# Kernel optimization log

Measured on AMD Instinct MI355X. Metric: run time of the kernel, lower is better.

The kernel has to match this reference:

```python
import jax, jax.numpy as jnp
import numpy as np

B, S, D, H = 2, 512, 1024, 8
DK = D // H
DFF = 4 * D
R = 51
SEP = 64


def setup_inputs() -> dict:
    key = jax.random.key(0)
    ks = jax.random.split(key, 12)
    def w(k, shape, scale=0.02):
        return jax.random.normal(k, shape, jnp.float32) * scale
    return {
        "x": jax.random.normal(ks[0], (B, S, D), jnp.float32),
        "relation": jax.random.randint(ks[1], (B, S, S), 0, R),
        "mask": jnp.ones((B, S, S), jnp.int32),
        "sep_id": SEP,
        "history_reg": jnp.ones((1,), jnp.float32),
        "Wq": w(ks[2], (D, D)), "bq": jnp.zeros((D,), jnp.float32),
        "Wk": w(ks[3], (D, D)), "bk": jnp.zeros((D,), jnp.float32),
        "Wv": w(ks[4], (D, D)), "bv": jnp.zeros((D,), jnp.float32),
        "Wo": w(ks[5], (D, D)), "bo": jnp.zeros((D,), jnp.float32),
        "rel_k_emb": w(ks[6], (R, DK)),
        "rel_v_emb": w(ks[7], (R, DK)),
        "ln1_g": jnp.ones((D,), jnp.float32), "ln1_b": jnp.zeros((D,), jnp.float32),
        "ln2_g": jnp.ones((D,), jnp.float32), "ln2_b": jnp.zeros((D,), jnp.float32),
        "W1": w(ks[8], (D, DFF)), "b1": jnp.zeros((DFF,), jnp.float32),
        "W2": w(ks[9], (DFF, D)), "b2": jnp.zeros((D,), jnp.float32),
    }


def _layer_norm(x, g, b, eps=1e-5):
    m = jnp.mean(x, axis=-1, keepdims=True)
    v = jnp.mean(jnp.square(x - m), axis=-1, keepdims=True)
    return (x - m) * jax.lax.rsqrt(v + eps) * g + b


def _forward(x, relation, mask, sep_id, history_reg, Wq, bq, Wk, bk, Wv, bv, Wo, bo,
             rel_k_emb, rel_v_emb, ln1_g, ln1_b, ln2_g, ln2_b, W1, b1, W2, b2):
    b, s, d = x.shape
    # relation-aware self-attention sublayer (pre-norm)
    h = _layer_norm(x, ln1_g, ln1_b)
    rk = rel_k_emb[relation]  # [B,S,S,DK]
    rv = rel_v_emb[relation]  # [B,S,S,DK]
    def proj(W, bias):
        return (h @ W + bias).reshape(b, s, H, DK).transpose(0, 2, 1, 3)  # [B,H,S,DK]
    q, k, v = proj(Wq, bq), proj(Wk, bk), proj(Wv, bv)
    scores = jnp.einsum("bhid,bhjd->bhij", q, k) + jnp.einsum("bhid,bijd->bhij", q, rk)
    scores = scores / jnp.sqrt(jnp.float32(DK))
    scores = jnp.where(mask[:, None, :, :] == 0, jnp.float32(-1e9), scores)
    attn = jax.nn.softmax(scores, axis=-1)  # [B,H,S,S]
    ctx = jnp.einsum("bhij,bhjd->bhid", attn, v) + jnp.einsum("bhij,bijd->bhid", attn, rv)
    ctx = ctx.transpose(0, 2, 1, 3).reshape(b, s, d)
    attn_out = ctx @ Wo + bo
    # history regularization loss: attention mass on history tokens (positions < sep_id)
    loss = history_reg[0] * jnp.mean(attn[:, :, :, :sep_id])
    x = x + attn_out
    # FFN sublayer (pre-norm)
    h2 = _layer_norm(x, ln2_g, ln2_b)
    ffn = jax.nn.relu(h2 @ W1 + b1) @ W2 + b2
    x = x + ffn
    return x, loss


def reference(x, relation, mask, sep_id, history_reg, Wq, bq, Wk, bk, Wv, bv, Wo, bo,
              rel_k_emb, rel_v_emb, ln1_g, ln1_b, ln2_g, ln2_b, W1, b1, W2, b2):
    return _forward(x, relation, mask, sep_id, history_reg, Wq, bq, Wk, bk, Wv, bv,
                    Wo, bo, rel_k_emb, rel_v_emb, ln1_g, ln1_b, ln2_g, ln2_b,
                    W1, b1, W2, b2)
```

## Files before the change

### kernel.cpp

```cpp
#include <hip/hip_runtime.h>
#include <hip/hip_bf16.h>

#define NB 2
#define NS 512
#define ND 1024
#define NH 8
#define NDK 128
#define NDFF 4096
#define RPAD 64
#define LDSC 640
#define BSROWS 1024
#define NBH 16

typedef __bf16 bf16x8 __attribute__((ext_vector_type(8)));
typedef __bf16 bf16x4 __attribute__((ext_vector_type(4)));
typedef float f32x4 __attribute__((ext_vector_type(4)));

#define BM 64
#define BN 64
#define BK 64

__device__ __forceinline__ void gload16(const void* g, void* l) {
    __builtin_amdgcn_global_load_lds(
        (const __attribute__((address_space(1))) void*)g,
        (__attribute__((address_space(3))) void*)l, 16, 0, 0);
}

__global__ __launch_bounds__(256, 4) void gemm64(
    const __bf16* __restrict__ A, const __bf16* __restrict__ Bt,
    const __bf16* __restrict__ Brel,
    float* __restrict__ Cf, __bf16* __restrict__ Cb,
    const float* __restrict__ bias,
    int Ksp, int lda, int ldb, int ldc,
    long sA, long sA2, int zdivA,
    long sB, long sB2, int zdivB,
    long sC, int nsplit, long sPart, int flags)
{
    __shared__ __bf16 As0[BM * BK];
    __shared__ __bf16 As1[BM * BK];
    __shared__ __bf16 Bs0[BN * BK];
    __shared__ __bf16 Bs1[BN * BK];

    const int z = blockIdx.z;
    const int bh = z / nsplit, sp = z - bh * nsplit;
    const long kbase = (long)sp * Ksp;
    A  += (long)(bh / zdivA) * sA + (long)(bh % zdivA) * sA2 + kbase;
    Bt += (long)(bh / zdivB) * sB + (long)(bh % zdivB) * sB2 + kbase;
    const long cbase = (long)bh * sC + (long)sp * sPart;

    const int tM = blockIdx.y * BM, tN = blockIdx.x * BN;
    const int t = threadIdx.x, lane = t & 63, w = t >> 6;
    const int wr = w >> 1, wc = w & 1;

    const __bf16* Bbase = Bt;
    int ldbx = ldb, tNB = tN;
    if ((flags & 4) && tN >= NS) { Bbase = Brel + kbase; ldbx = 128; tNB = tN - NS; }

    const int srow = lane >> 3;
    const int scolE = ((((lane & 7) << 4) ^ (srow << 4)) >> 1);

    const __bf16* gA = A + (long)(tM + srow) * lda + scolE;
    const __bf16* gB = Bbase + (long)(tNB + srow) * ldbx + scolE;

    f32x4 acc[2][2];
#pragma unroll
    for (int m = 0; m < 2; ++m)
#pragma unroll
        for (int n = 0; n < 2; ++n)
#pragma unroll
            for (int j = 0; j < 4; ++j) acc[m][n][j] = 0.f;

    const int r16 = lane & 15;
    const int kq = (lane >> 4) * 8;
    const int xorE = (r16 & 7) * 8;
    const int nt = Ksp / BK;

    auto STAGE = [&](__bf16* as, __bf16* bs, int k0) {
#pragma unroll
        for (int i = 0; i < 2; ++i) {
            const int rr = (w + i * 4) * 8;
            gload16(gA + (long)rr * lda + k0, (void*)&as[rr * BK]);
            gload16(gB + (long)rr * ldbx + k0, (void*)&bs[rr * BK]);
        }
    };
    auto COMPUTE = [&](const __bf16* as, const __bf16* bs) {
#pragma unroll
        for (int ks = 0; ks < 2; ++ks) {
            bf16x8 af[2], bv[2];
#pragma unroll
            for (int m = 0; m < 2; ++m)
                af[m] = *(const bf16x8*)&as[(wr * 32 + m * 16 + r16) * BK + ((ks * 32 + kq) ^ xorE)];
#pragma unroll
            for (int n = 0; n < 2; ++n)
                bv[n] = *(const bf16x8*)&bs[(wc * 32 + n * 16 + r16) * BK + ((ks * 32 + kq) ^ xorE)];
#pragma unroll
            for (int m = 0; m < 2; ++m)
#pragma unroll
                for (int n = 0; n < 2; ++n)
                    acc[m][n] = __builtin_amdgcn_mfma_f32_16x16x32_bf16(af[m], bv[n], acc[m][n], 0, 0, 0);
        }
    };

    STAGE(As0, Bs0, 0);
    STAGE(As1, Bs1, BK);
    for (int tt = 0; tt < nt; tt += 2) {
        asm volatile("s_waitcnt vmcnt(4)\n\ts_barrier" ::: "memory");
        COMPUTE(As0, Bs0);
        asm volatile("s_waitcnt lgkmcnt(0)\n\ts_barrier" ::: "memory");
        const bool more = (tt + 2 < nt);
        if (more) {
            STAGE(As0, Bs0, (tt + 2) * BK);
            asm volatile("s_waitcnt vmcnt(4)\n\ts_barrier" ::: "memory");
        } else {
            asm volatile("s_waitcnt vmcnt(0)\n\ts_barrier" ::: "memory");
        }
        COMPUTE(As1, Bs1);
        asm volatile("s_waitcnt lgkmcnt(0)\n\ts_barrier" ::: "memory");
        if (more) STAGE(As1, Bs1, (tt + 3) * BK);
    }

    const bool relu = (flags & 1) != 0;
#pragma unroll
    for (int m = 0; m < 2; ++m) {
        const int gr0 = tM + wr * 32 + m * 16 + (lane >> 4) * 4;
#pragma unroll
        for (int n = 0; n < 2; ++n) {
            const int gc = tN + wc * 32 + n * 16 + (lane & 15);
            const float bb = bias ? bias[gc] : 0.f;
#pragma unroll
            for (int j = 0; j < 4; ++j) {
                float v = acc[m][n][j] + bb;
                if (relu) v = fmaxf(v, 0.f);
                const long idx = cbase + (long)(gr0 + j) * ldc + gc;
                if (Cb) Cb[idx] = (__bf16)v;
                else Cf[idx] = v;
            }
        }
    }
}

__global__ __launch_bounds__(256) void ln_bf16(
    const float* __restrict__ x, const float* __restrict__ g,
    const float* __restrict__ bb, __bf16* __restrict__ out)
{
    const long row = blockIdx.x;
    const float* xr = x + row * ND;
    __bf16* orow = out + row * ND;
    const int t = threadIdx.x;
    float4 v = reinterpret_cast<const float4*>(xr)[t];
    float s = v.x + v.y + v.z + v.w;
    float s2 = v.x * v.x + v.y * v.y + v.z * v.z + v.w * v.w;
#pragma unroll
    for (int o = 32; o > 0; o >>= 1) {
        s += __shfl_xor(s, o, 64);
        s2 += __shfl_xor(s2, o, 64);
    }
    __shared__ float red[8];
    const int lane = t & 63, wv = t >> 6;
    if (lane == 0) { red[wv] = s; red[4 + wv] = s2; }
    __syncthreads();
    s = red[0] + red[1] + red[2] + red[3];
    s2 = red[4] + red[5] + red[6] + red[7];
    const float mean = s * (1.f / ND);
    const float var = s2 * (1.f / ND) - mean * mean;
    const float rs = rsqrtf(var + 1e-5f);
    const float xv[4] = {v.x, v.y, v.z, v.w};
    bf16x4 o;
#pragma unroll
    for (int j = 0; j < 4; ++j) {
        const int c = t * 4 + j;
        o[j] = (__bf16)((xv[j] - mean) * rs * g[c] + bb[c]);
    }
    *(bf16x4*)&orow[t * 4] = o;
}

__global__ void prep_weights(
    const float* __restrict__ Wq, const float* __restrict__ Wk,
    const float* __restrict__ Wv, const float* __restrict__ Wo,
    const float* __restrict__ W1, const float* __restrict__ W2,
    const float* __restrict__ relv,
    const float* __restrict__ bq, const float* __restrict__ bk,
    const float* __restrict__ bv, const float* __restrict__ relk,
    __bf16* __restrict__ WqkvT, __bf16* __restrict__ WoT,
    __bf16* __restrict__ W1T, __bf16* __restrict__ W2T,
    __bf16* __restrict__ relvT, float* __restrict__ biasqkv,
    __bf16* __restrict__ relkT, int R)
{
    const int tile = blockIdx.x;
    if (tile >= 12296) {
        const int ft = (tile - 12296) * 256 + threadIdx.y * 32 + threadIdx.x;
        if (ft < ND) biasqkv[ft] = bq[ft];
        else if (ft < 2 * ND) biasqkv[ft] = bk[ft - ND];
        else if (ft < 3 * ND) biasqkv[ft] = bv[ft - 2 * ND];
        else {
            const int idx = ft - 3 * ND;
            if (idx < 128 * NDK) {
                const int r = idx / NDK;
                relkT[idx] = (r < R) ? (__bf16)relk[idx] : (__bf16)0.f;
            }
        }
        return;
    }
    const float* src; __bf16* dst;
    int rows_in, cols_in, ldo, kx, ny;
    if (tile < 4096) {
        const int m = tile >> 10, r = tile & 1023;
        kx = r & 31; ny = r >> 5;
        rows_in = 1024; cols_in = 1024; ldo = 1024;
        src = m == 0 ? Wq : m == 1 ? Wk : m == 2 ? Wv : Wo;
        dst = m == 3 ? WoT : WqkvT + (size_t)m * 1024 * 1024;
    } else if (tile < 8192) {
        const int r = tile - 4096;
        kx = r & 31; ny = r >> 5;
        rows_in = 1024; cols_in = 4096; ldo = 1024; src = W1; dst = W1T;
    } else if (tile < 12288) {
        const int r = tile - 8192;
        kx = r & 127; ny = r >> 7;
        rows_in = 4096; cols_in = 1024; ldo = 4096; src = W2; dst = W2T;
    } else {
        const int r = tile - 12288;
        kx = r & 1; ny = r >> 1;
        rows_in = R; cols_in = 128; ldo = 64; src = relv; dst = relvT;
    }

    __shared__ float tl[32][33];
    const int k0 = kx * 32, n0 = ny * 32;
    const int tx = threadIdx.x, ty = threadIdx.y;
#pragma unroll
    for (int dy = 0; dy < 32; dy += 8) {
        const int k = k0 + ty + dy, n = n0 + tx;
        tl[ty + dy][tx] = (k < rows_in && n < cols_in) ? src[(long)k * cols_in + n] : 0.f;
    }
    __syncthreads();
#pragma unroll
    for (int dy = 0; dy < 32; dy += 8) {
        const int n = n0 + ty + dy, k = k0 + tx;
        if (n < cols_in && k < ldo) dst[(long)n * ldo + k] = (__bf16)tl[tx][ty + dy];
    }
}

__global__ void transpose_v(const __bf16* __restrict__ qkvb, __bf16* __restrict__ vt)
{
    __shared__ __bf16 tile[32][33];
    const int bh = blockIdx.z, b = bh >> 3, h = bh & 7;
    const int d0 = blockIdx.x * 32, i0 = blockIdx.y * 32;
    const int tx = threadIdx.x, ty = threadIdx.y;
    const __bf16* src = qkvb + 2 * ND + h * NDK;
#pragma unroll
    for (int dy = 0; dy < 32; dy += 8)
        tile[ty + dy][tx] = src[(long)(b * NS + i0 + ty + dy) * (3 * ND) + d0 + tx];
    __syncthreads();
#pragma unroll
    for (int dy = 0; dy < 32; dy += 8)
        vt[((long)bh * NDK + d0 + ty + dy) * NS + i0 + tx] = tile[tx][ty + dy];
}

__global__ __launch_bounds__(256) void softmax_rel(
    const __bf16* __restrict__ scores,
    const int* __restrict__ relation, const int* __restrict__ mask,
    __bf16* __restrict__ attn, __bf16* __restrict__ attnR,
    float* __restrict__ loss_part, const int* __restrict__ sep_p)
{
    const int i = blockIdx.x, b = blockIdx.y;
    const int t = threadIdx.x;
    const int* rrow = relation + ((long)b * NS + i) * NS;
    const int* mrow = mask + ((long)b * NS + i) * NS;
    const int r0 = rrow[t], r1 = rrow[t + 256];
    const int m0 = mrow[t], m1 = mrow[t + 256];
    const int sep = *sep_p;
    const int lane = t & 63, wv = t >> 6;

    __shared__ float qrl[RPAD];
    __shared__ float bins[RPAD];
    __shared__ float red[4];

    const float sc = 0.088388347648318447f;
    float lsum = 0.f;

#pragma unroll 1
    for (int h = 0; h < NH; ++h) {
        const long bh = (long)(b * NH + h);
        const __bf16* srow = scores + (bh * NS + i) * LDSC;
        __bf16* arow = attn + (bh * NS + i) * NS;
        __bf16* aRrow = attnR + (bh * NS + i) * RPAD;

        if (t < RPAD) { qrl[t] = (float)srow[NS + t]; bins[t] = 0.f; }
        __syncthreads();

        float v0 = ((float)srow[t] + qrl[r0]) * sc;
        float v1 = ((float)srow[t + 256] + qrl[r1]) * sc;
        if (m0 == 0) v0 = -1e9f;
        if (m1 == 0) v1 = -1e9f;

        float mx = fmaxf(v0, v1);
#pragma unroll
        for (int o = 32; o > 0; o >>= 1) mx = fmaxf(mx, __shfl_xor(mx, o, 64));
        if (lane == 0) red[wv] = mx;
        __syncthreads();
        mx = fmaxf(fmaxf(red[0], red[1]), fmaxf(red[2], red[3]));
        __syncthreads();

        const float e0 = __expf(v0 - mx), e1 = __expf(v1 - mx);
        float sm = e0 + e1;
#pragma unroll
        for (int o = 32; o > 0; o >>= 1) sm += __shfl_xor(sm, o, 64);
        if (lane == 0) red[wv] = sm;
        __syncthreads();
        sm = red[0] + red[1] + red[2] + red[3];

        const float inv = 1.f / sm;
        const float a0 = e0 * inv, a1 = e1 * inv;
        arow[t] = (__bf16)a0;
        arow[t + 256] = (__bf16)a1;
        atomicAdd(&bins[r0], a0);
        atomicAdd(&bins[r1], a1);
        if (t < sep) lsum += a0;
        if (t + 256 < sep) lsum += a1;
        __syncthreads();
        if (t < RPAD) aRrow[t] = (__bf16)bins[t];
        __syncthreads();
    }

#pragma unroll
    for (int o = 32; o > 0; o >>= 1) lsum += __shfl_xor(lsum, o, 64);
    if (lane == 0) red[wv] = lsum;
    __syncthreads();
    if (t == 0) loss_part[(long)b * NS + i] = red[0] + red[1] + red[2] + red[3];
}

__global__ __launch_bounds__(256) void ctx_reduce(
    const float* __restrict__ P, const __bf16* __restrict__ attnR,
    const __bf16* __restrict__ relvT, __bf16* __restrict__ ctxm)
{
    const int idx = blockIdx.x * 256 + threadIdx.x;
    const int d = idx & 127;
    const int i = (idx >> 7) & 511;
    const int h = (idx >> 16) & 7;
    const int b = idx >> 19;
    const long sP = (long)NBH * NS * NDK;
    float s = P[idx] + P[idx + sP];

    const bf16x8* ar = (const bf16x8*)(attnR + ((long)(idx >> 16) * NS + i) * RPAD);
    const bf16x8* rv = (const bf16x8*)(relvT + (long)d * RPAD);
    float acc = 0.f;
#pragma unroll
    for (int q = 0; q < 8; ++q) {
        bf16x8 a = ar[q], vv = rv[q];
#pragma unroll
        for (int j = 0; j < 8; ++j) acc += (float)a[j] * (float)vv[j];
    }
    ctxm[((long)(b * NS + i)) * ND + h * NDK + d] = (__bf16)(s + acc);
}

__global__ __launch_bounds__(256) void wo_reduce_ln(
    const float* __restrict__ P, const float* __restrict__ x,
    const float* __restrict__ bo, const float* __restrict__ g,
    const float* __restrict__ bb, float* __restrict__ out,
    __bf16* __restrict__ h2)
{
    const int row = blockIdx.x;
    const int t = threadIdx.x;
    const long i4 = (long)row * 256 + t;
    const long sP = (long)BSROWS * ND / 4;
    const float4* P4 = (const float4*)P;
    float4 s = P4[i4];
    const float4 t1 = P4[i4 + sP];
    s.x += t1.x; s.y += t1.y; s.z += t1.z; s.w += t1.w;
    const int col = t * 4;
    const float4 xv = ((const float4*)x)[i4];
    const float4 bv = *(const float4*)&bo[col];
    float4 o;
    o.x = s.x + xv.x + bv.x; o.y = s.y + xv.y + bv.y;
    o.z = s.z + xv.z + bv.z; o.w = s.w + xv.w + bv.w;
    ((float4*)out)[i4] = o;

    float sum = o.x + o.y + o.z + o.w;
    float sum2 = o.x * o.x + o.y * o.y + o.z * o.z + o.w * o.w;
#pragma unroll
    for (int of = 32; of > 0; of >>= 1) {
        sum += __shfl_xor(sum, of, 64);
        sum2 += __shfl_xor(sum2, of, 64);
    }
    __shared__ float red[8];
    const int lane = t & 63, wv = t >> 6;
    if (lane == 0) { red[wv] = sum; red[4 + wv] = sum2; }
    __syncthreads();
    sum = red[0] + red[1] + red[2] + red[3];
    sum2 = red[4] + red[5] + red[6] + red[7];
    const float mean = sum * (1.f / ND);
    const float var = sum2 * (1.f / ND) - mean * mean;
    const float rs = rsqrtf(var + 1e-5f);
    const float ov[4] = {o.x, o.y, o.z, o.w};
    bf16x4 hb;
#pragma unroll
    for (int j = 0; j < 4; ++j)
        hb[j] = (__bf16)((ov[j] - mean) * rs * g[col + j] + bb[col + j]);
    *(bf16x4*)&h2[(long)row * ND + col] = hb;
}

__global__ __launch_bounds__(256) void ffn2_reduce(
    const float* __restrict__ P, const float* __restrict__ b2, float* __restrict__ out,
    const float* __restrict__ loss_part, const float* __restrict__ hist,
    const int* __restrict__ sep_p, float* __restrict__ out_loss)
{
    const int i4 = blockIdx.x * 256 + threadIdx.x;
    const long sP = (long)BSROWS * ND / 4;
    const float4* P4 = (const float4*)P;
    float4 s = P4[i4];
    const float4 t1 = P4[i4 + sP];
    s.x += t1.x; s.y += t1.y; s.z += t1.z; s.w += t1.w;
    const int col = (i4 * 4) & (ND - 1);
    const float4 bv = *(const float4*)&b2[col];
    float4 o = ((float4*)out)[i4];
    o.x += s.x + bv.x; o.y += s.y + bv.y;
    o.z += s.z + bv.z; o.w += s.w + bv.w;
    ((float4*)out)[i4] = o;

    if (blockIdx.x == 0) {
        const int t = threadIdx.x;
        const float4 v = ((const float4*)loss_part)[t];
        float ls = v.x + v.y + v.z + v.w;
#pragma unroll
        for (int of = 32; of > 0; of >>= 1) ls += __shfl_xor(ls, of, 64);
        __shared__ float red[4];
        if ((t & 63) == 0) red[t >> 6] = ls;
        __syncthreads();
        if (t == 0) {
            const int sep = *sep_p;
            const float total = red[0] + red[1] + red[2] + red[3];
            const float denom = (float)NB * NH * NS * (float)(sep > 0 ? sep : 1);
            out_loss[0] = (sep > 0) ? hist[0] * total / denom : 0.f;
        }
    }
}

static inline int cdiv(int a, int b) { return (a + b - 1) / b; }

extern "C" void kernel_launch(void* const* d_in, const int* in_sizes, int n_in,
                              void* d_out, int out_size, void* d_ws, size_t ws_size,
                              hipStream_t stream)
{
    const float* x      = (const float*)d_in[0];
    const int* relation = (const int*)d_in[1];
    const int* mask     = (const int*)d_in[2];
    const int* sep_p    = (const int*)d_in[3];
    const float* hist   = (const float*)d_in[4];
    const float* Wq = (const float*)d_in[5],  *bq = (const float*)d_in[6];
    const float* Wk = (const float*)d_in[7],  *bk = (const float*)d_in[8];
    const float* Wv = (const float*)d_in[9],  *bv = (const float*)d_in[10];
    const float* Wo = (const float*)d_in[11], *bo = (const float*)d_in[12];
    const float* relk = (const float*)d_in[13];
    const float* relv = (const float*)d_in[14];
    const float* ln1g = (const float*)d_in[15], *ln1b = (const float*)d_in[16];
    const float* ln2g = (const float*)d_in[17], *ln2b = (const float*)d_in[18];
    const float* W1 = (const float*)d_in[19], *b1 = (const float*)d_in[20];
    const float* W2 = (const float*)d_in[21], *b2 = (const float*)d_in[22];
    const int R = in_sizes[13] / NDK;

    float* out = (float*)d_out;
    float* out_loss = out + (long)BSROWS * ND;

    char* p = (char*)d_ws;
    auto alloc = [&](size_t bytes) -> void* {
        void* r = (void*)p;
        p += (bytes + 255) & ~(size_t)255;
        return r;
    };
    __bf16* WqkvT   = (__bf16*)alloc((size_t)3 * ND * ND * 2);
    __bf16* WoT     = (__bf16*)alloc((size_t)ND * ND * 2);
    __bf16* W1T     = (__bf16*)alloc((size_t)NDFF * ND * 2);
    __bf16* W2T     = (__bf16*)alloc((size_t)ND * NDFF * 2);
    __bf16* relkT   = (__bf16*)alloc((size_t)128 * NDK * 2);
    __bf16* relvT   = (__bf16*)alloc((size_t)NDK * RPAD * 2);
    float*  biasqkv = (float*)alloc((size_t)3 * ND * 4);
    __bf16* h1      = (__bf16*)alloc((size_t)BSROWS * ND * 2);
    __bf16* qkvb    = (__bf16*)alloc((size_t)BSROWS * 3 * ND * 2);
    __bf16* vt      = (__bf16*)alloc((size_t)NBH * NDK * NS * 2);
    __bf16* attnb   = (__bf16*)alloc((size_t)NBH * NS * NS * 2);
    __bf16* attnR   = (__bf16*)alloc((size_t)NBH * NS * RPAD * 2);
    __bf16* ctxm    = (__bf16*)alloc((size_t)BSROWS * ND * 2);
    __bf16* h2      = (__bf16*)alloc((size_t)BSROWS * ND * 2);
    __bf16* F1      = (__bf16*)alloc((size_t)BSROWS * NDFF * 2);
    float*  loss_part = (float*)alloc((size_t)NB * NS * 4);
    float*  arena   = (float*)alloc((size_t)64 * 1024 * 1024);
    __bf16* scoresb = (__bf16*)arena;
    float* ctxPart  = arena + (size_t)3 * 1024 * 1024;
    float* woPart   = arena;
    float* f2Part   = arena + (size_t)2 * 1024 * 1024;

    const dim3 tb(32, 8);
    prep_weights<<<12372, tb, 0, stream>>>(Wq, Wk, Wv, Wo, W1, W2, relv,
                                           bq, bk, bv, relk,
                                           WqkvT, WoT, W1T, W2T, relvT,
                                           biasqkv, relkT, R);

    ln_bf16<<<BSROWS, 256, 0, stream>>>(x, ln1g, ln1b, h1);

    gemm64<<<dim3(48, 16, 1), 256, 0, stream>>>(
        h1, WqkvT, nullptr, nullptr, qkvb, biasqkv,
        ND, ND, ND, 3 * ND,
        0, 0, 1, 0, 0, 1, 0, 1, 0, 0);

    transpose_v<<<dim3(4, 16, NBH), tb, 0, stream>>>(qkvb, vt);

    gemm64<<<dim3(10, 8, NBH), 256, 0, stream>>>(
        qkvb, qkvb + ND, relkT, nullptr, scoresb, nullptr,
        NDK, 3 * ND, 3 * ND, LDSC,
        (long)NS * 3 * ND, NDK, NH,
        (long)NS * 3 * ND, NDK, NH,
        (long)NS * LDSC, 1, 0, 4);

    softmax_rel<<<dim3(NS, NB), 256, 0, stream>>>(
        scoresb, relation, mask, attnb, attnR, loss_part, sep_p);

    gemm64<<<dim3(2, 8, NBH * 2), 256, 0, stream>>>(
        attnb, vt, nullptr, ctxPart, nullptr, nullptr,
        256, NS, NS, NDK,
        (long)NS * NS, 0, 1,
        (long)NDK * NS, 0, 1,
        (long)NS * NDK, 2, (long)NBH * NS * NDK, 0);

    ctx_reduce<<<4096, 256, 0, stream>>>(ctxPart, attnR, relvT, ctxm);

    gemm64<<<dim3(16, 16, 2), 256, 0, stream>>>(
        ctxm, WoT, nullptr, woPart, nullptr, nullptr,
        512, ND, ND, ND,
        0, 0, 1, 0, 0, 1,
        0, 2, (long)BSROWS * ND, 0);

    wo_reduce_ln<<<BSROWS, 256, 0, stream>>>(woPart, x, bo, ln2g, ln2b, out, h2);

    gemm64<<<dim3(64, 16, 1), 256, 0, stream>>>(
        h2, W1T, nullptr, nullptr, F1, b1,
        ND, ND, ND, NDFF,
        0, 0, 1, 0, 0, 1, 0, 1, 0, 1);

    gemm64<<<dim3(16, 16, 2), 256, 0, stream>>>(
        F1, W2T, nullptr, f2Part, nullptr, nullptr,
        2048, NDFF, NDFF, ND,
        0, 0, 1, 0, 0, 1,
        0, 2, (long)BSROWS * ND, 0);

    ffn2_reduce<<<1024, 256, 0, stream>>>(f2Part, b2, out,
                                          loss_part, hist, sep_p, out_loss);
}
```

Baseline: 162.7 us.

## Fuse LN1 into prep kernel, remap GEMM blocks per XCD, raise MFMA priority

Folds the first layer norm into the weight-prep kernel as extra blocks, which removes one kernel launch. The GEMM's block index is remapped so consecutive logical tiles land on the same XCD, aiming for better L2 reuse on the multi-die MI355X. It also wraps the MFMA compute section in s_setprio to favour matrix issue. The remap adds integer division per block, and the fused prep kernel now shares its LDS layout between two different code paths.

```diff
diff --git a/kernel.cpp b/kernel.cpp
--- a/kernel.cpp
+++ b/kernel.cpp
@@ -41,14 +41,22 @@
     __shared__ __bf16 Bs0[BN * BK];
     __shared__ __bf16 Bs1[BN * BK];
 
-    const int z = blockIdx.z;
+    const unsigned gx = gridDim.x, gy = gridDim.y;
+    const unsigned n = gx * gy * gridDim.z;
+    const unsigned o = blockIdx.x + gx * (blockIdx.y + gy * blockIdx.z);
+    const unsigned q = n >> 3, r = n & 7, xcd = o & 7;
+    const unsigned nl = (xcd < r ? xcd * (q + 1) : r * (q + 1) + (xcd - r) * q) + (o >> 3);
+    const unsigned bx = nl % gx, tmp = nl / gx;
+    const unsigned by = tmp % gy, bz = tmp / gy;
+
+    const int z = bz;
     const int bh = z / nsplit, sp = z - bh * nsplit;
     const long kbase = (long)sp * Ksp;
     A  += (long)(bh / zdivA) * sA + (long)(bh % zdivA) * sA2 + kbase;
     Bt += (long)(bh / zdivB) * sB + (long)(bh % zdivB) * sB2 + kbase;
     const long cbase = (long)bh * sC + (long)sp * sPart;
 
-    const int tM = blockIdx.y * BM, tN = blockIdx.x * BN;
+    const int tM = by * BM, tN = bx * BN;
     const int t = threadIdx.x, lane = t & 63, w = t >> 6;
     const int wr = w >> 1, wc = w & 1;
 
@@ -66,9 +74,9 @@
 #pragma unroll
     for (int m = 0; m < 2; ++m)
 #pragma unroll
-        for (int n = 0; n < 2; ++n)
-#pragma unroll
-            for (int j = 0; j < 4; ++j) acc[m][n][j] = 0.f;
+        for (int nn = 0; nn < 2; ++nn)
+#pragma unroll
+            for (int j = 0; j < 4; ++j) acc[m][nn][j] = 0.f;
 
     const int r16 = lane & 15;
     const int kq = (lane >> 4) * 8;
@@ -84,6 +92,7 @@
         }
     };
     auto COMPUTE = [&](const __bf16* as, const __bf16* bs) {
+        __builtin_amdgcn_s_setprio(1);
 #pragma unroll
         for (int ks = 0; ks < 2; ++ks) {
             bf16x8 af[2], bv[2];
@@ -91,14 +100,15 @@
             for (int m = 0; m < 2; ++m)
                 af[m] = *(const bf16x8*)&as[(wr * 32 + m * 16 + r16) * BK + ((ks * 32 + kq) ^ xorE)];
 #pragma unroll
-            for (int n = 0; n < 2; ++n)
-                bv[n] = *(const bf16x8*)&bs[(wc * 32 + n * 16 + r16) * BK + ((ks * 32 + kq) ^ xorE)];
+            for (int nn = 0; nn < 2; ++nn)
+                bv[nn] = *(const bf16x8*)&bs[(wc * 32 + nn * 16 + r16) * BK + ((ks * 32 + kq) ^ xorE)];
 #pragma unroll
             for (int m = 0; m < 2; ++m)
 #pragma unroll
-                for (int n = 0; n < 2; ++n)
-                    acc[m][n] = __builtin_amdgcn_mfma_f32_16x16x32_bf16(af[m], bv[n], acc[m][n], 0, 0, 0);
-        }
+                for (int nn = 0; nn < 2; ++nn)
+                    acc[m][nn] = __builtin_amdgcn_mfma_f32_16x16x32_bf16(af[m], bv[nn], acc[m][nn], 0, 0, 0);
+        }
+        __builtin_amdgcn_s_setprio(0);
     };
 
     STAGE(As0, Bs0, 0);
@@ -124,12 +134,12 @@
     for (int m = 0; m < 2; ++m) {
         const int gr0 = tM + wr * 32 + m * 16 + (lane >> 4) * 4;
 #pragma unroll
-        for (int n = 0; n < 2; ++n) {
-            const int gc = tN + wc * 32 + n * 16 + (lane & 15);
+        for (int nn = 0; nn < 2; ++nn) {
+            const int gc = tN + wc * 32 + nn * 16 + (lane & 15);
             const float bb = bias ? bias[gc] : 0.f;
 #pragma unroll
             for (int j = 0; j < 4; ++j) {
-                float v = acc[m][n][j] + bb;
+                float v = acc[m][nn][j] + bb;
                 if (relu) v = fmaxf(v, 0.f);
                 const long idx = cbase + (long)(gr0 + j) * ldc + gc;
                 if (Cb) Cb[idx] = (__bf16)v;
@@ -137,41 +147,6 @@
             }
         }
     }
-}
-
-__global__ __launch_bounds__(256) void ln_bf16(
-    const float* __restrict__ x, const float* __restrict__ g,
-    const float* __restrict__ bb, __bf16* __restrict__ out)
-{
-    const long row = blockIdx.x;
-    const float* xr = x + row * ND;
-    __bf16* orow = out + row * ND;
-    const int t = threadIdx.x;
-    float4 v = reinterpret_cast<const float4*>(xr)[t];
-    float s = v.x + v.y + v.z + v.w;
-    float s2 = v.x * v.x + v.y * v.y + v.z * v.z + v.w * v.w;
-#pragma unroll
-    for (int o = 32; o > 0; o >>= 1) {
-        s += __shfl_xor(s, o, 64);
-        s2 += __shfl_xor(s2, o, 64);
-    }
-    __shared__ float red[8];
-    const int lane = t & 63, wv = t >> 6;
-    if (lane == 0) { red[wv] = s; red[4 + wv] = s2; }
-    __syncthreads();
-    s = red[0] + red[1] + red[2] + red[3];
-    s2 = red[4] + red[5] + red[6] + red[7];
-    const float mean = s * (1.f / ND);
-    const float var = s2 * (1.f / ND) - mean * mean;
-    const float rs = rsqrtf(var + 1e-5f);
-    const float xv[4] = {v.x, v.y, v.z, v.w};
-    bf16x4 o;
-#pragma unroll
-    for (int j = 0; j < 4; ++j) {
-        const int c = t * 4 + j;
-        o[j] = (__bf16)((xv[j] - mean) * rs * g[c] + bb[c]);
-    }
-    *(bf16x4*)&orow[t * 4] = o;
 }
 
 __global__ void prep_weights(
@@ -181,14 +156,48 @@
     const float* __restrict__ relv,
     const float* __restrict__ bq, const float* __restrict__ bk,
     const float* __restrict__ bv, const float* __restrict__ relk,
+    const float* __restrict__ x, const float* __restrict__ ln1g,
+    const float* __restrict__ ln1b,
     __bf16* __restrict__ WqkvT, __bf16* __restrict__ WoT,
     __bf16* __restrict__ W1T, __bf16* __restrict__ W2T,
     __bf16* __restrict__ relvT, float* __restrict__ biasqkv,
-    __bf16* __restrict__ relkT, int R)
+    __bf16* __restrict__ relkT, __bf16* __restrict__ h1, int R)
 {
     const int tile = blockIdx.x;
+    const int t = threadIdx.y * 32 + threadIdx.x;
+
+    if (tile >= 12372) {
+        const long row = tile - 12372;
+        const float* xr = x + row * ND;
+        float4 v = reinterpret_cast<const float4*>(xr)[t];
+        float s = v.x + v.y + v.z + v.w;
+        float s2 = v.x * v.x + v.y * v.y + v.z * v.z + v.w * v.w;
+#pragma unroll
+        for (int o = 32; o > 0; o >>= 1) {
+            s += __shfl_xor(s, o, 64);
+            s2 += __shfl_xor(s2, o, 64);
+        }
+        __shared__ float red[8];
+        const int lane = t & 63, wv = t >> 6;
+        if (lane == 0) { red[wv] = s; red[4 + wv] = s2; }
+        __syncthreads();
+        s = red[0] + red[1] + red[2] + red[3];
+        s2 = red[4] + red[5] + red[6] + red[7];
+        const float mean = s * (1.f / ND);
+        const float var = s2 * (1.f / ND) - mean * mean;
+        const float rs = rsqrtf(var + 1e-5f);
+        const float xv[4] = {v.x, v.y, v.z, v.w};
+        bf16x4 o;
+#pragma unroll
+        for (int j = 0; j < 4; ++j) {
+            const int c = t * 4 + j;
+            o[j] = (__bf16)((xv[j] - mean) * rs * ln1g[c] + ln1b[c]);
+        }
+        *(bf16x4*)&h1[row * ND + t * 4] = o;
+        return;
+    }
     if (tile >= 12296) {
-        const int ft = (tile - 12296) * 256 + threadIdx.y * 32 + threadIdx.x;
+        const int ft = (tile - 12296) * 256 + t;
         if (ft < ND) biasqkv[ft] = bq[ft];
         else if (ft < 2 * ND) biasqkv[ft] = bk[ft - ND];
         else if (ft < 3 * ND) biasqkv[ft] = bv[ft - 2 * ND];
@@ -228,14 +237,14 @@
     const int tx = threadIdx.x, ty = threadIdx.y;
 #pragma unroll
     for (int dy = 0; dy < 32; dy += 8) {
-        const int k = k0 + ty + dy, n = n0 + tx;
-        tl[ty + dy][tx] = (k < rows_in && n < cols_in) ? src[(long)k * cols_in + n] : 0.f;
+        const int k = k0 + ty + dy, nn = n0 + tx;
+        tl[ty + dy][tx] = (k < rows_in && nn < cols_in) ? src[(long)k * cols_in + nn] : 0.f;
     }
     __syncthreads();
 #pragma unroll
     for (int dy = 0; dy < 32; dy += 8) {
-        const int n = n0 + ty + dy, k = k0 + tx;
-        if (n < cols_in && k < ldo) dst[(long)n * ldo + k] = (__bf16)tl[tx][ty + dy];
+        const int nn = n0 + ty + dy, k = k0 + tx;
+        if (nn < cols_in && k < ldo) dst[(long)nn * ldo + k] = (__bf16)tl[tx][ty + dy];
     }
 }
 
@@ -489,12 +498,10 @@
     float* f2Part   = arena + (size_t)2 * 1024 * 1024;
 
     const dim3 tb(32, 8);
-    prep_weights<<<12372, tb, 0, stream>>>(Wq, Wk, Wv, Wo, W1, W2, relv,
-                                           bq, bk, bv, relk,
+    prep_weights<<<13396, tb, 0, stream>>>(Wq, Wk, Wv, Wo, W1, W2, relv,
+                                           bq, bk, bv, relk, x, ln1g, ln1b,
                                            WqkvT, WoT, W1T, W2T, relvT,
-                                           biasqkv, relkT, R);
-
-    ln_bf16<<<BSROWS, 256, 0, stream>>>(x, ln1g, ln1b, h1);
+                                           biasqkv, relkT, h1, R);
 
     gemm64<<<dim3(48, 16, 1), 256, 0, stream>>>(
         h1, WqkvT, nullptr, nullptr, qkvb, biasqkv,
```

Measured after the change: 162.2 us. Within noise of the previous version (-0.3%).
